# Kernel tuning notes

Measured on AMD Instinct MI355X. Metric: run time of the kernel, lower is better.

The kernel has to match this reference:

```python
import jax, jax.numpy as jnp
import numpy as np

# Hamilton product tables: out component q uses weight IDX[q,p] with sign SGN[q,p]
# applied to input component p. Components order: (r, i, j, k); weights order: (rr, ri, rj, rk).
IDX = np.array([[0, 1, 2, 3], [1, 0, 3, 2], [2, 3, 0, 1], [3, 2, 1, 0]])
SGN = np.array([[1., -1., -1., -1.], [1., 1., 1., -1.], [1., -1., 1., 1.], [1., 1., -1., 1.]], dtype=np.float32)


def _qlinear(x4, w, b):
    # x4: (B, 4, Cin4, H, W); w: (4, Cout4, Cin4); b: (4, Cout4)
    # Quaternion 1x1 conv == channel-mixing matmul with Hamilton sign structure.
    wstk = jnp.asarray(SGN)[:, :, None, None] * w[IDX]  # (4,4,Cout4,Cin4)
    out = jnp.einsum('qpoc,bpchw->bqohw', wstk, x4)
    return out + b[None, :, :, None, None]


def _qdwconv(x4, w, b):
    # x4: (B, 4, Cc, H, W); w: (4, Cc, 1, 3, 3) depthwise per-channel; b: (4, Cc)
    Cc = x4.shape[2]
    comps = [x4[:, p] for p in range(4)]  # each (B, Cc, H, W)
    outs = []
    for qc in range(4):
        acc = None
        for p in range(4):
            c = SGN[qc, p] * jax.lax.conv_general_dilated(
                comps[p], w[IDX[qc, p]], window_strides=(1, 1), padding='SAME',
                feature_group_count=Cc, dimension_numbers=('NCHW', 'OIHW', 'NCHW'))
            acc = c if acc is None else acc + c
        outs.append(acc + b[qc][None, :, None, None])
    return jnp.stack(outs, axis=1)  # (B, 4, Cc, H, W)


def setup_inputs() -> dict:
    key = jax.random.key(0)
    ks = jax.random.split(key, 4)
    B, Cc, H, W = 8, 256, 32, 32   # dim = 4*Cc = 1024
    dim = 4 * Cc
    num_heads, key_dim = 8, 128
    h = 3 * num_heads * key_dim    # 3072 total -> 768 per component
    x = jax.random.normal(ks[0], (B, Cc, 4, H, W), jnp.float32)
    w_qkv = jax.random.normal(ks[1], (4, h // 4, dim // 4), jnp.float32) * (1.0 / np.sqrt(dim))
    b_qkv = jnp.zeros((4, h // 4), jnp.float32)
    w_proj = jax.random.normal(ks[2], (4, dim // 4, dim // 4), jnp.float32) * (1.0 / np.sqrt(dim))
    b_proj = jnp.zeros((4, dim // 4), jnp.float32)
    w_pe = jax.random.normal(ks[3], (4, dim // 4, 1, 3, 3), jnp.float32) * (1.0 / 6.0)
    b_pe = jnp.zeros((4, dim // 4), jnp.float32)
    return {'x': x, 'w_qkv': w_qkv, 'b_qkv': b_qkv, 'w_proj': w_proj,
            'b_proj': b_proj, 'w_pe': w_pe, 'b_pe': b_pe}


def reference(x, w_qkv, b_qkv, w_proj, b_proj, w_pe, b_pe):
    B, Cc, Q, H, W = x.shape
    num_heads, key_dim = 8, 128
    scale = key_dim ** -0.5
    N = H * W
    xq = jnp.transpose(x, (0, 2, 1, 3, 4))            # (B, 4, Cc, H, W)
    qkv = _qlinear(xq, w_qkv, b_qkv)                  # (B, 4, 768, H, W)
    q4, k4, v4 = jnp.split(qkv, 3, axis=2)            # each (B, 4, 256, H, W)

    def to_heads(t):  # (B,4,Cc,H,W) -> (B, heads, key_dim, N)
        return t.reshape(B, 4 * Cc, N).reshape(B, num_heads, key_dim, N)

    q, k, v = to_heads(q4), to_heads(k4), to_heads(v4)
    scores = jnp.einsum('bhdn,bhdm->bhnm', q, k) * scale   # (B,H,N,N) fully materialized
    attn = jax.nn.softmax(scores, axis=-1)
    out = jnp.einsum('bhnm,bhdm->bhdn', attn, v)           # (B,H,key_dim,N)
    out4 = out.reshape(B, 4, Cc, H, W)
    out = _qlinear(out4, w_proj, b_proj) + _qdwconv(xq, w_pe, b_pe)
    return jnp.transpose(out, (0, 2, 1, 3, 4))             # (B, Cc, 4, H, W)
```

## Files before the change

### kernel.cpp

```cpp
#include <hip/hip_runtime.h>
#include <hip/hip_bf16.h>

typedef unsigned short u16;
typedef float f32x4 __attribute__((ext_vector_type(4)));
typedef __bf16 bf16x8 __attribute__((ext_vector_type(8)));
typedef unsigned short su8v __attribute__((ext_vector_type(8)));
typedef unsigned short su4v __attribute__((ext_vector_type(4)));

#define BB 8
#define NHD 8
#define DD 128
#define NN 1024
#define DIM 1024
#define H3 3072
#define MM 8192
#define PTS 72
#define QSC (0.08838834764831845f * 1.4426950408889634f)

__constant__ int   d_IDX[16] = {0,1,2,3, 1,0,3,2, 2,3,0,1, 3,2,1,0};
__constant__ float d_SGN[16] = {1.f,-1.f,-1.f,-1.f, 1.f,1.f,1.f,-1.f,
                                1.f,-1.f,1.f,1.f,  1.f,1.f,-1.f,1.f};

__device__ __forceinline__ f32x4 mfma16(su8v a, su8v b, f32x4 c) {
  return __builtin_amdgcn_mfma_f32_16x16x32_bf16(
      __builtin_bit_cast(bf16x8, a), __builtin_bit_cast(bf16x8, b), c, 0, 0, 0);
}
__device__ __forceinline__ u16 f2b(float f) {
  unsigned int u = __builtin_bit_cast(unsigned int, f);
  u += 0x7fffu + ((u >> 16) & 1u);
  return (u16)(u >> 16);
}
__device__ __forceinline__ float b2f(u16 v) {
  unsigned int u = ((unsigned int)v) << 16;
  return __builtin_bit_cast(float, u);
}
typedef const __attribute__((address_space(1))) unsigned int* gas_t;
typedef __attribute__((address_space(3))) unsigned int* las_t;
__device__ __forceinline__ void gll16(const u16* g, u16* l) {
  __builtin_amdgcn_global_load_lds((gas_t)g, (las_t)l, 16, 0, 0);
}

__global__ __launch_bounds__(256) void prep_weff(
    const float* __restrict__ wqkv, const float* __restrict__ wproj,
    u16* __restrict__ weffQ, u16* __restrict__ weffP) {
  int tid = blockIdx.x * 256 + threadIdx.x;
  int stride = gridDim.x * 256;
  for (int i = tid; i < H3 * DIM; i += stride) {
    int row = i >> 10, col = i & 1023;
    int q = row / 768, o = row - q * 768;
    int p = col >> 8, c = col & 255;
    float v = d_SGN[q * 4 + p] * wqkv[(d_IDX[q * 4 + p] * 768 + o) * 256 + c];
    if (o < 256) v *= QSC;
    weffQ[i] = f2b(v);
  }
  for (int i = tid; i < DIM * DIM; i += stride) {
    int row = i >> 10, col = i & 1023;
    int q = row >> 8, o = row & 255;
    int p = col >> 8, c = col & 255;
    weffP[i] = f2b(d_SGN[q * 4 + p] * wproj[(d_IDX[q * 4 + p] * 256 + o) * 256 + c]);
  }
}

__global__ __launch_bounds__(256) void prep_x(
    const float* __restrict__ x, u16* __restrict__ Ax) {
  int id = blockIdx.x * 256 + threadIdx.x;
  const float4* xv = (const float4*)x;
  float4 f = xv[id];
  int n4 = id & 255;
  int rem = id >> 8;
  int p = rem & 3, c = (rem >> 2) & 255, b = rem >> 10;
  int col = p * 256 + c;
  size_t rbase = (size_t)(b * 1024 + n4 * 4) * 1024 + col;
  Ax[rbase] = f2b(f.x);
  Ax[rbase + 1024] = f2b(f.y);
  Ax[rbase + 2048] = f2b(f.z);
  Ax[rbase + 3072] = f2b(f.w);
}

__device__ __forceinline__ void gemm_core2(
    const u16* __restrict__ Ag, const u16* __restrict__ Bg,
    u16* As, u16* Bs, int tid, f32x4 acc[4][4]) {
  int w = tid >> 6, lane = tid & 63, l16 = lane & 15, quad = lane >> 4;
  int mt = (w & 1) * 64, nt = (w >> 1) * 64;
  int srow = lane >> 3;
  int scol = ((lane & 7) ^ srow) * 8;
  int x7 = l16 & 7;
  for (int k0 = 0; k0 < 1024; k0 += 64) {
    __syncthreads();
#pragma unroll
    for (int t = 0; t < 4; ++t) {
      int ci = w * 4 + t;
      int row = ci * 8 + srow;
      gll16(Ag + (size_t)row * 1024 + k0 + scol, As + ci * 512);
      gll16(Bg + (size_t)row * 1024 + k0 + scol, Bs + ci * 512);
    }
    __syncthreads();
#pragma unroll
    for (int kk = 0; kk < 2; ++kk) {
      su8v af[4], bf[4];
#pragma unroll
      for (int i = 0; i < 4; ++i)
        af[i] = *(const su8v*)(As + (mt + i * 16 + l16) * 64 +
                               ((kk * 4 + quad) ^ x7) * 8);
#pragma unroll
      for (int j = 0; j < 4; ++j)
        bf[j] = *(const su8v*)(Bs + (nt + j * 16 + l16) * 64 +
                               ((kk * 4 + quad) ^ x7) * 8);
#pragma unroll
      for (int i = 0; i < 4; ++i)
#pragma unroll
        for (int j = 0; j < 4; ++j)
          acc[i][j] = mfma16(af[i], bf[j], acc[i][j]);
    }
  }
}

__global__ __launch_bounds__(256) void gemm_qkv_mfma(
    const u16* __restrict__ Ax, const u16* __restrict__ weffQ,
    const float* __restrict__ bqkv,
    u16* __restrict__ Qb, u16* __restrict__ Kb, u16* __restrict__ VbT) {
  __shared__ u16 As[128 * 64];
  __shared__ u16 Bs[128 * 64];
  int m0 = blockIdx.x * 128;
  int col0 = blockIdx.y * 128;
  int qq = col0 / 768;
  int off = col0 - qq * 768;
  int sel = off >> 8;
  int head = (qq * 256 + (off & 255)) >> 7;
  int tid = threadIdx.x;
  int w = tid >> 6, lane = tid & 63, l16 = lane & 15, quad = lane >> 4;
  int mt = (w & 1) * 64, nt = (w >> 1) * 64;
  f32x4 acc[4][4];
#pragma unroll
  for (int i = 0; i < 4; ++i)
#pragma unroll
    for (int j = 0; j < 4; ++j) acc[i][j] = (f32x4){0.f, 0.f, 0.f, 0.f};

  if (sel == 2) {
    gemm_core2(Ax + (size_t)m0 * 1024, weffQ + (size_t)col0 * 1024, As, Bs,
               tid, acc);
#pragma unroll
    for (int j = 0; j < 4; ++j) {
      int d = nt + j * 16 + l16;
      float bias = bqkv[col0 + nt + j * 16 + l16];
#pragma unroll
      for (int i = 0; i < 4; ++i) {
        int m = m0 + mt + i * 16 + quad * 4;
        int b = m >> 10, npos = m & 1023;
        int bh = b * NHD + head;
        su4v pk;
#pragma unroll
        for (int r = 0; r < 4; ++r) pk[r] = f2b(acc[i][j][r] + bias);
        *(su4v*)(VbT + ((size_t)bh * DD + d) * NN + npos) = pk;
      }
    }
  } else {
    gemm_core2(weffQ + (size_t)col0 * 1024, Ax + (size_t)m0 * 1024, As, Bs,
               tid, acc);
    u16* dst = (sel == 0) ? Qb : Kb;
    float sc = (sel == 0) ? (float)QSC : 1.0f;
#pragma unroll
    for (int i = 0; i < 4; ++i) {
      int dbase = mt + i * 16 + quad * 4;
      float4 b4 = *(const float4*)(bqkv + col0 + dbase);
#pragma unroll
      for (int j = 0; j < 4; ++j) {
        int nglob = m0 + nt + j * 16 + l16;
        int b = nglob >> 10, npos = nglob & 1023;
        int bh = b * NHD + head;
        su4v pk;
        pk[0] = f2b(acc[i][j][0] + b4.x * sc);
        pk[1] = f2b(acc[i][j][1] + b4.y * sc);
        pk[2] = f2b(acc[i][j][2] + b4.z * sc);
        pk[3] = f2b(acc[i][j][3] + b4.w * sc);
        *(su4v*)(dst + ((size_t)bh * NN + npos) * DD + dbase) = pk;
      }
    }
  }
}

__global__ __launch_bounds__(256) void attn_mfma(
    const u16* __restrict__ Qb, const u16* __restrict__ Kb,
    const u16* __restrict__ VbT, u16* __restrict__ OP,
    float* __restrict__ LS) {
  __shared__ u16 Ks[64 * 128];
  __shared__ u16 Vt[128 * 64];
  __shared__ u16 Ps[4 * 32 * PTS];
  int blk = blockIdx.x;
  int bh = blk & 63;
  int rest = blk >> 6;
  int qt = rest & 7;
  int half = rest >> 3;
  int n0 = qt * 128;
  int tid = threadIdx.x;
  int w = tid >> 6, lane = tid & 63, l16 = lane & 15, quad = lane >> 4;
  const u16* Qg = Qb + ((size_t)bh * NN + n0) * DD;
  const u16* Kg = Kb + (size_t)bh * NN * DD;
  const u16* Vg = VbT + (size_t)bh * DD * NN;
  u16* Pw = Ps + w * 32 * PTS;
  int x7 = l16 & 7;

  su8v qreg[2][4];
#pragma unroll
  for (int mi = 0; mi < 2; ++mi)
#pragma unroll
    for (int ch = 0; ch < 4; ++ch)
      qreg[mi][ch] = *(const su8v*)(Qg + (size_t)(w * 32 + mi * 16 + l16) * DD +
                                    ch * 32 + quad * 8);

  float ls[2] = {0.f, 0.f};
  f32x4 accO[2][8];
#pragma unroll
  for (int mi = 0; mi < 2; ++mi)
#pragma unroll
    for (int dt = 0; dt < 8; ++dt) accO[mi][dt] = (f32x4){0.f, 0.f, 0.f, 0.f};

  for (int kt = 0; kt < 8; ++kt) {
    int c0 = half * 512 + kt * 64;
    __syncthreads();
#pragma unroll
    for (int t = 0; t < 4; ++t) {
      int ci = w * 4 + t;
      int krow = ci * 4 + (lane >> 4);
      int kblk = (lane & 15) ^ (krow & 7);
      gll16(Kg + (size_t)(c0 + krow) * DD + kblk * 8, Ks + ci * 512);
      int dv = ci * 8 + (lane >> 3);
      int vblk = (lane & 7) ^ (dv & 7);
      gll16(Vg + (size_t)dv * NN + c0 + vblk * 8, Vt + ci * 512);
    }
    __syncthreads();

    f32x4 sacc[2][4];
#pragma unroll
    for (int mi = 0; mi < 2; ++mi)
#pragma unroll
      for (int j = 0; j < 4; ++j) sacc[mi][j] = (f32x4){0.f, 0.f, 0.f, 0.f};
#pragma unroll
    for (int j = 0; j < 4; ++j) {
#pragma unroll
      for (int ch = 0; ch < 4; ++ch) {
        su8v kf = *(const su8v*)(Ks + (j * 16 + l16) * 128 +
                                 (((ch * 4 + quad) ^ x7) * 8));
        sacc[0][j] = mfma16(kf, qreg[0][ch], sacc[0][j]);
        sacc[1][j] = mfma16(kf, qreg[1][ch], sacc[1][j]);
      }
    }

#pragma unroll
    for (int mi = 0; mi < 2; ++mi)
#pragma unroll
      for (int j = 0; j < 4; ++j) {
        su4v pk;
#pragma unroll
        for (int r = 0; r < 4; ++r) {
          float p = __builtin_exp2f(sacc[mi][j][r]);
          ls[mi] += p;
          pk[r] = (u16)(__builtin_bit_cast(unsigned int, p) >> 16);
        }
        *(su4v*)(Pw + (mi * 16 + l16) * PTS + j * 16 + quad * 4) = pk;
      }

#pragma unroll
    for (int ch = 0; ch < 2; ++ch) {
      su8v pf0 = *(const su8v*)(Pw + l16 * PTS + ch * 32 + quad * 8);
      su8v pf1 = *(const su8v*)(Pw + (16 + l16) * PTS + ch * 32 + quad * 8);
#pragma unroll
      for (int dt = 0; dt < 8; ++dt) {
        su8v vf = *(const su8v*)(Vt + (dt * 16 + l16) * 64 +
                                 (((ch * 4 + quad) ^ x7) * 8));
        accO[0][dt] = mfma16(pf0, vf, accO[0][dt]);
        accO[1][dt] = mfma16(pf1, vf, accO[1][dt]);
      }
    }
  }

#pragma unroll
  for (int mi = 0; mi < 2; ++mi) {
    float s = ls[mi];
    s += __shfl_xor(s, 16, 64);
    s += __shfl_xor(s, 32, 64);
    ls[mi] = s;
  }
  size_t hb = (size_t)(half * 64 + bh);
  if (quad == 0) {
#pragma unroll
    for (int mi = 0; mi < 2; ++mi)
      LS[hb * NN + n0 + w * 32 + mi * 16 + l16] = ls[mi];
  }
#pragma unroll
  for (int mi = 0; mi < 2; ++mi)
#pragma unroll
    for (int r = 0; r < 4; ++r) {
      int row = w * 32 + mi * 16 + quad * 4 + r;
      size_t base = (hb * NN + n0 + row) * DD;
#pragma unroll
      for (int dt = 0; dt < 8; ++dt)
        OP[base + dt * 16 + l16] = f2b(accO[mi][dt][r]);
    }
}

__global__ __launch_bounds__(256) void attn_merge(
    const u16* __restrict__ OP, const float* __restrict__ LS,
    u16* __restrict__ AO) {
  size_t idx = (size_t)blockIdx.x * 256 + threadIdx.x;
  size_t e = idx * 4;
  int d = (int)(e & 127);
  size_t bhn = e >> 7;
  su4v a = *(const su4v*)(OP + bhn * DD + d);
  su4v b = *(const su4v*)(OP + (size_t)64 * NN * DD + bhn * DD + d);
  float inv = 1.0f / (LS[bhn] + LS[bhn + 64 * NN]);
  int bh = (int)(bhn >> 10), n = (int)(bhn & 1023);
  int bb = bh >> 3, head = bh & 7;
  su4v o;
#pragma unroll
  for (int r = 0; r < 4; ++r) o[r] = f2b((b2f(a[r]) + b2f(b[r])) * inv);
  *(su4v*)(AO + ((size_t)(bb * 1024 + n) * 1024) + head * 128 + d) = o;
}

__global__ __launch_bounds__(256) void qdwconv_kernel(
    const float* __restrict__ x, const float* __restrict__ wpe,
    const float* __restrict__ bpe, float* __restrict__ pe) {
  int blk = blockIdx.x;
  int co = blk & 255;
  int b = blk >> 8;
  __shared__ float pl[4][34 * 34];
  __shared__ float wsm[4][9];
  int tid = threadIdx.x;
  for (int i = tid; i < 4 * 34 * 34; i += 256) ((float*)pl)[i] = 0.f;
  if (tid < 36) wsm[tid / 9][tid % 9] = wpe[((tid / 9) * 256 + co) * 9 + tid % 9];
  __syncthreads();
  for (int i = tid; i < 4 * 1024; i += 256) {
    int p = i >> 10, n = i & 1023;
    int h = n >> 5, ww = n & 31;
    pl[p][(h + 1) * 34 + (ww + 1)] =
        x[(((size_t)b * 256 + co) * 4 + p) * 1024 + n];
  }
  __syncthreads();
  for (int n = tid; n < 1024; n += 256) {
    int h = n >> 5, ww = n & 31;
    float in[4][9];
#pragma unroll
    for (int p = 0; p < 4; ++p)
#pragma unroll
      for (int t = 0; t < 9; ++t)
        in[p][t] = pl[p][(h + t / 3) * 34 + (ww + t % 3)];
#pragma unroll
    for (int q = 0; q < 4; ++q) {
      float acc = bpe[q * 256 + co];
#pragma unroll
      for (int p = 0; p < 4; ++p) {
        int idx = d_IDX[q * 4 + p];
        float s = d_SGN[q * 4 + p];
        float sub = 0.f;
#pragma unroll
        for (int t = 0; t < 9; ++t) sub += in[p][t] * wsm[idx][t];
        acc += s * sub;
      }
      pe[(((size_t)b * 256 + co) * 4 + q) * 1024 + n] = acc;
    }
  }
}

__global__ __launch_bounds__(256) void gemm_proj_mfma(
    const u16* __restrict__ AO, const u16* __restrict__ weffP,
    const float* __restrict__ bproj, const float* __restrict__ pe,
    float* __restrict__ out) {
  __shared__ u16 As[128 * 64];
  __shared__ u16 Bs[128 * 64];
  int n0 = blockIdx.x * 128;
  int m0 = blockIdx.y * 128;
  int tid = threadIdx.x;
  f32x4 acc[4][4];
#pragma unroll
  for (int i = 0; i < 4; ++i)
#pragma unroll
    for (int j = 0; j < 4; ++j) acc[i][j] = (f32x4){0.f, 0.f, 0.f, 0.f};
  gemm_core2(weffP + (size_t)m0 * 1024, AO + (size_t)n0 * 1024, As, Bs, tid, acc);

  int w = tid >> 6, lane = tid & 63, l16 = lane & 15, quad = lane >> 4;
  int mt = (w & 1) * 64, nt = (w >> 1) * 64;
#pragma unroll
  for (int i = 0; i < 4; ++i) {
#pragma unroll
    for (int r = 0; r < 4; ++r) {
      int mrow = m0 + mt + i * 16 + quad * 4 + r;
      int q = mrow >> 8, o = mrow & 255;
      float bias = bproj[mrow];
#pragma unroll
      for (int j = 0; j < 4; ++j) {
        int n = n0 + nt + j * 16 + l16;
        int b = n >> 10, npos = n & 1023;
        size_t oidx = (((size_t)b * 256 + o) * 4 + q) * 1024 + npos;
        out[oidx] = pe[oidx] + acc[i][j][r] + bias;
      }
    }
  }
}

extern "C" void kernel_launch(void* const* d_in, const int* in_sizes, int n_in,
                              void* d_out, int out_size, void* d_ws,
                              size_t ws_size, hipStream_t stream) {
  const float* x      = (const float*)d_in[0];
  const float* w_qkv  = (const float*)d_in[1];
  const float* b_qkv  = (const float*)d_in[2];
  const float* w_proj = (const float*)d_in[3];
  const float* b_proj = (const float*)d_in[4];
  const float* w_pe   = (const float*)d_in[5];
  const float* b_pe   = (const float*)d_in[6];
  float* out = (float*)d_out;

  u16* ws = (u16*)d_ws;
  u16* weffQ = ws;
  u16* weffP = weffQ + (size_t)H3 * DIM;
  u16* Ax    = weffP + (size_t)DIM * DIM;
  u16* Qb    = Ax + (size_t)MM * DIM;
  u16* Kb    = Qb + (size_t)BB * NHD * NN * DD;
  u16* VbT   = Kb + (size_t)BB * NHD * NN * DD;
  u16* AO    = VbT + (size_t)BB * NHD * DD * NN;
  float* PE  = (float*)(AO + (size_t)MM * DIM);
  u16* OP    = (u16*)(PE + (size_t)MM * DIM);
  float* LS  = (float*)(OP + (size_t)2 * 64 * NN * DD);

  hipLaunchKernelGGL(prep_weff, dim3(4096), dim3(256), 0, stream,
                     w_qkv, w_proj, weffQ, weffP);
  hipLaunchKernelGGL(prep_x, dim3(8192), dim3(256), 0, stream, x, Ax);
  hipLaunchKernelGGL(gemm_qkv_mfma, dim3(MM / 128, H3 / 128), dim3(256), 0,
                     stream, Ax, weffQ, b_qkv, Qb, Kb, VbT);
  hipLaunchKernelGGL(attn_mfma, dim3(1024), dim3(256), 0, stream,
                     Qb, Kb, VbT, OP, LS);
  hipLaunchKernelGGL(attn_merge, dim3((64 * NN * DD) / (256 * 4)), dim3(256),
                     0, stream, OP, LS, AO);
  hipLaunchKernelGGL(qdwconv_kernel, dim3(BB * 256), dim3(256), 0, stream,
                     x, w_pe, b_pe, PE);
  hipLaunchKernelGGL(gemm_proj_mfma, dim3(MM / 128, DIM / 128), dim3(256), 0,
                     stream, AO, weffP, b_proj, PE, out);
}
```

Baseline: 318.5 us.

## Triple-buffer GEMM tiles with async prefetch and larger 256x128 blocks

Replaces the synchronous single-buffer GEMM core with a templated triple-buffered pipeline. It prefetches the A and B tiles two k-steps ahead, using vmcnt waits, split barriers and s_setprio around the MFMA bursts. The QKV and projection GEMMs move to 512-thread blocks covering 256x128 tiles, with launch grids halved to match. This is meant to hide global-load latency and raise data reuse per block, at the cost of larger LDS use (about 144KB per block) and more register pressure, which may limit occupancy.

New measurement: 318.2 us. No clear change (-0.1%).

```diff
diff --git a/kernel.cpp b/kernel.cpp
--- a/kernel.cpp
+++ b/kernel.cpp
@@ -77,59 +77,111 @@
   Ax[rbase + 3072] = f2b(f.w);
 }
 
-__device__ __forceinline__ void gemm_core2(
+template <int BM, int BN>
+__device__ __forceinline__ void gemm_core8(
     const u16* __restrict__ Ag, const u16* __restrict__ Bg,
-    u16* As, u16* Bs, int tid, f32x4 acc[4][4]) {
+    u16* As, u16* Bs, int tid, f32x4 (&acc)[4][4]) {
+  constexpr int WN = BN / 64;
+  constexpr int AC = BM / 64;
+  constexpr int BC = BN / 64;
+  constexpr int NT = 16;
   int w = tid >> 6, lane = tid & 63, l16 = lane & 15, quad = lane >> 4;
-  int mt = (w & 1) * 64, nt = (w >> 1) * 64;
+  int wm = w / WN, wn = w % WN;
+  int x7 = l16 & 7;
   int srow = lane >> 3;
-  int scol = ((lane & 7) ^ srow) * 8;
-  int x7 = l16 & 7;
-  for (int k0 = 0; k0 < 1024; k0 += 64) {
-    __syncthreads();
-#pragma unroll
-    for (int t = 0; t < 4; ++t) {
-      int ci = w * 4 + t;
-      int row = ci * 8 + srow;
-      gll16(Ag + (size_t)row * 1024 + k0 + scol, As + ci * 512);
-      gll16(Bg + (size_t)row * 1024 + k0 + scol, Bs + ci * 512);
-    }
-    __syncthreads();
-#pragma unroll
-    for (int kk = 0; kk < 2; ++kk) {
+  int sblk = (lane & 7) ^ srow;
+
+  auto STAGE_A = [&](int tt, int bs) {
+#pragma unroll
+    for (int c = 0; c < AC; ++c) {
+      int r0 = c * 64 + w * 8;
+      gll16(Ag + (size_t)(r0 + srow) * 1024 + tt * 64 + sblk * 8,
+            As + (size_t)bs * (BM * 64) + r0 * 64);
+    }
+  };
+  auto STAGE_B = [&](int tt, int bs) {
+#pragma unroll
+    for (int c = 0; c < BC; ++c) {
+      int r0 = c * 64 + w * 8;
+      gll16(Bg + (size_t)(r0 + srow) * 1024 + tt * 64 + sblk * 8,
+            Bs + (size_t)bs * (BN * 64) + r0 * 64);
+    }
+  };
+
+  STAGE_A(0, 0); STAGE_B(0, 0);
+  STAGE_A(1, 1); STAGE_B(1, 1);
+  asm volatile("s_waitcnt vmcnt(6)" ::: "memory");
+  __builtin_amdgcn_s_barrier();
+
+  int cur = 0, nxt = 1, stg = 2;
+  for (int t = 0; t < NT; ++t) {
+    const u16* At = As + (size_t)cur * (BM * 64);
+    const u16* Bt = Bs + (size_t)cur * (BN * 64);
+    {
       su8v af[4], bf[4];
 #pragma unroll
       for (int i = 0; i < 4; ++i)
-        af[i] = *(const su8v*)(As + (mt + i * 16 + l16) * 64 +
-                               ((kk * 4 + quad) ^ x7) * 8);
+        af[i] = *(const su8v*)(At + (wm * 64 + i * 16 + l16) * 64 +
+                               (quad ^ x7) * 8);
 #pragma unroll
       for (int j = 0; j < 4; ++j)
-        bf[j] = *(const su8v*)(Bs + (nt + j * 16 + l16) * 64 +
-                               ((kk * 4 + quad) ^ x7) * 8);
+        bf[j] = *(const su8v*)(Bt + (wn * 64 + j * 16 + l16) * 64 +
+                               (quad ^ x7) * 8);
+      if (t + 2 < NT) STAGE_A(t + 2, stg);
+      asm volatile("" ::: "memory");
+      __builtin_amdgcn_s_barrier();
+      __builtin_amdgcn_s_setprio(1);
 #pragma unroll
       for (int i = 0; i < 4; ++i)
 #pragma unroll
         for (int j = 0; j < 4; ++j)
           acc[i][j] = mfma16(af[i], bf[j], acc[i][j]);
-    }
-  }
-}
-
-__global__ __launch_bounds__(256) void gemm_qkv_mfma(
+      __builtin_amdgcn_s_setprio(0);
+      asm volatile("" ::: "memory");
+      __builtin_amdgcn_s_barrier();
+    }
+    {
+      su8v af[4], bf[4];
+#pragma unroll
+      for (int i = 0; i < 4; ++i)
+        af[i] = *(const su8v*)(At + (wm * 64 + i * 16 + l16) * 64 +
+                               ((4 + quad) ^ x7) * 8);
+#pragma unroll
+      for (int j = 0; j < 4; ++j)
+        bf[j] = *(const su8v*)(Bt + (wn * 64 + j * 16 + l16) * 64 +
+                               ((4 + quad) ^ x7) * 8);
+      if (t + 2 < NT) STAGE_B(t + 2, stg);
+      asm volatile("" ::: "memory");
+      __builtin_amdgcn_s_barrier();
+      __builtin_amdgcn_s_setprio(1);
+#pragma unroll
+      for (int i = 0; i < 4; ++i)
+#pragma unroll
+        for (int j = 0; j < 4; ++j)
+          acc[i][j] = mfma16(af[i], bf[j], acc[i][j]);
+      __builtin_amdgcn_s_setprio(0);
+      if (t < NT - 2)       asm volatile("s_waitcnt vmcnt(6)" ::: "memory");
+      else if (t == NT - 2) asm volatile("s_waitcnt vmcnt(0)" ::: "memory");
+      asm volatile("" ::: "memory");
+      __builtin_amdgcn_s_barrier();
+    }
+    int tmp = cur; cur = nxt; nxt = stg; stg = tmp;
+  }
+}
+
+__global__ __launch_bounds__(512, 2) void gemm_qkv_mfma(
     const u16* __restrict__ Ax, const u16* __restrict__ weffQ,
     const float* __restrict__ bqkv,
     u16* __restrict__ Qb, u16* __restrict__ Kb, u16* __restrict__ VbT) {
-  __shared__ u16 As[128 * 64];
-  __shared__ u16 Bs[128 * 64];
-  int m0 = blockIdx.x * 128;
+  __shared__ u16 smem[3 * 384 * 64];
+  int bn0 = blockIdx.x * 256;
   int col0 = blockIdx.y * 128;
-  int qq = col0 / 768;
-  int off = col0 - qq * 768;
+  int q = col0 / 768;
+  int off = col0 - q * 768;
   int sel = off >> 8;
-  int head = (qq * 256 + (off & 255)) >> 7;
+  int head = (q * 256 + (off & 255)) >> 7;
   int tid = threadIdx.x;
   int w = tid >> 6, lane = tid & 63, l16 = lane & 15, quad = lane >> 4;
-  int mt = (w & 1) * 64, nt = (w >> 1) * 64;
   f32x4 acc[4][4];
 #pragma unroll
   for (int i = 0; i < 4; ++i)
@@ -137,36 +189,38 @@
     for (int j = 0; j < 4; ++j) acc[i][j] = (f32x4){0.f, 0.f, 0.f, 0.f};
 
   if (sel == 2) {
-    gemm_core2(Ax + (size_t)m0 * 1024, weffQ + (size_t)col0 * 1024, As, Bs,
-               tid, acc);
+    gemm_core8<256, 128>(Ax + (size_t)bn0 * 1024, weffQ + (size_t)col0 * 1024,
+                         smem, smem + 3 * 256 * 64, tid, acc);
+    int wm = w >> 1, wn = w & 1;
 #pragma unroll
     for (int j = 0; j < 4; ++j) {
-      int d = nt + j * 16 + l16;
-      float bias = bqkv[col0 + nt + j * 16 + l16];
+      int dl = wn * 64 + j * 16 + l16;
+      float bias = bqkv[col0 + dl];
 #pragma unroll
       for (int i = 0; i < 4; ++i) {
-        int m = m0 + mt + i * 16 + quad * 4;
+        int m = bn0 + wm * 64 + i * 16 + quad * 4;
         int b = m >> 10, npos = m & 1023;
         int bh = b * NHD + head;
         su4v pk;
 #pragma unroll
         for (int r = 0; r < 4; ++r) pk[r] = f2b(acc[i][j][r] + bias);
-        *(su4v*)(VbT + ((size_t)bh * DD + d) * NN + npos) = pk;
+        *(su4v*)(VbT + ((size_t)bh * DD + dl) * NN + npos) = pk;
       }
     }
   } else {
-    gemm_core2(weffQ + (size_t)col0 * 1024, Ax + (size_t)m0 * 1024, As, Bs,
-               tid, acc);
+    gemm_core8<128, 256>(weffQ + (size_t)col0 * 1024, Ax + (size_t)bn0 * 1024,
+                         smem, smem + 3 * 128 * 64, tid, acc);
+    int wm = w >> 2, wn = w & 3;
     u16* dst = (sel == 0) ? Qb : Kb;
     float sc = (sel == 0) ? (float)QSC : 1.0f;
 #pragma unroll
     for (int i = 0; i < 4; ++i) {
-      int dbase = mt + i * 16 + quad * 4;
+      int dbase = wm * 64 + i * 16 + quad * 4;
       float4 b4 = *(const float4*)(bqkv + col0 + dbase);
 #pragma unroll
       for (int j = 0; j < 4; ++j) {
-        int nglob = m0 + nt + j * 16 + l16;
-        int b = nglob >> 10, npos = nglob & 1023;
+        int n = bn0 + wn * 64 + j * 16 + l16;
+        int b = n >> 10, npos = n & 1023;
         int bh = b * NHD + head;
         su4v pk;
         pk[0] = f2b(acc[i][j][0] + b4.x * sc);
@@ -361,13 +415,12 @@
   }
 }
 
-__global__ __launch_bounds__(256) void gemm_proj_mfma(
+__global__ __launch_bounds__(512, 2) void gemm_proj_mfma(
     const u16* __restrict__ AO, const u16* __restrict__ weffP,
     const float* __restrict__ bproj, const float* __restrict__ pe,
     float* __restrict__ out) {
-  __shared__ u16 As[128 * 64];
-  __shared__ u16 Bs[128 * 64];
-  int n0 = blockIdx.x * 128;
+  __shared__ u16 smem[3 * 384 * 64];
+  int n0 = blockIdx.x * 256;
   int m0 = blockIdx.y * 128;
   int tid = threadIdx.x;
   f32x4 acc[4][4];
@@ -375,20 +428,21 @@
   for (int i = 0; i < 4; ++i)
 #pragma unroll
     for (int j = 0; j < 4; ++j) acc[i][j] = (f32x4){0.f, 0.f, 0.f, 0.f};
-  gemm_core2(weffP + (size_t)m0 * 1024, AO + (size_t)n0 * 1024, As, Bs, tid, acc);
+  gemm_core8<128, 256>(weffP + (size_t)m0 * 1024, AO + (size_t)n0 * 1024,
+                       smem, smem + 3 * 128 * 64, tid, acc);
 
   int w = tid >> 6, lane = tid & 63, l16 = lane & 15, quad = lane >> 4;
-  int mt = (w & 1) * 64, nt = (w >> 1) * 64;
+  int wm = w >> 2, wn = w & 3;
 #pragma unroll
   for (int i = 0; i < 4; ++i) {
 #pragma unroll
     for (int r = 0; r < 4; ++r) {
-      int mrow = m0 + mt + i * 16 + quad * 4 + r;
+      int mrow = m0 + wm * 64 + i * 16 + quad * 4 + r;
       int q = mrow >> 8, o = mrow & 255;
       float bias = bproj[mrow];
 #pragma unroll
       for (int j = 0; j < 4; ++j) {
-        int n = n0 + nt + j * 16 + l16;
+        int n = n0 + wn * 64 + j * 16 + l16;
         int b = n >> 10, npos = n & 1023;
         size_t oidx = (((size_t)b * 256 + o) * 4 + q) * 1024 + npos;
         out[oidx] = pe[oidx] + acc[i][j][r] + bias;
@@ -424,7 +478,7 @@
   hipLaunchKernelGGL(prep_weff, dim3(4096), dim3(256), 0, stream,
                      w_qkv, w_proj, weffQ, weffP);
   hipLaunchKernelGGL(prep_x, dim3(8192), dim3(256), 0, stream, x, Ax);
-  hipLaunchKernelGGL(gemm_qkv_mfma, dim3(MM / 128, H3 / 128), dim3(256), 0,
+  hipLaunchKernelGGL(gemm_qkv_mfma, dim3(MM / 256, H3 / 128), dim3(512), 0,
                      stream, Ax, weffQ, b_qkv, Qb, Kb, VbT);
   hipLaunchKernelGGL(attn_mfma, dim3(1024), dim3(256), 0, stream,
                      Qb, Kb, VbT, OP, LS);
@@ -432,6 +486,6 @@
                      0, stream, OP, LS, AO);
   hipLaunchKernelGGL(qdwconv_kernel, dim3(BB * 256), dim3(256), 0, stream,
                      x, w_pe, b_pe, PE);
-  hipLaunchKernelGGL(gemm_proj_mfma, dim3(MM / 128, DIM / 128), dim3(256), 0,
+  hipLaunchKernelGGL(gemm_proj_mfma, dim3(MM / 256, DIM / 128), dim3(512), 0,
                      stream, AO, weffP, b_proj, PE, out);
 }
```
